# Performance work log

Measured on AMD Instinct MI355X. Metric: run time of the kernel, lower is better.

Reference implementation:

```python
import jax, jax.numpy as jnp
import numpy as np

N, E, D, R = 50000, 800000, 64, 8
NEG_SLOPE = 0.2
EPS = 1e-9


def setup_inputs() -> dict:
    key = jax.random.key(0)
    k1, k2, k3, k4, k5, k6 = jax.random.split(key, 6)
    h = jax.random.normal(k1, (N, D), dtype=jnp.float32)
    W = jax.random.normal(k2, (R, D, D), dtype=jnp.float32) / np.sqrt(D)
    a = jax.random.normal(k3, (R, 2 * D), dtype=jnp.float32) * 0.1
    dropout_mask = jnp.ones((D,), dtype=jnp.float32)
    src = jax.random.randint(k4, (E,), 0, N, dtype=jnp.int32)
    dst = jax.random.randint(k5, (E,), 0, N, dtype=jnp.int32)
    etype = jax.random.randint(k6, (E,), 0, R, dtype=jnp.int32)
    return {"h": h, "W": W, "a": a, "dropout_mask": dropout_mask,
            "src": src, "dst": dst, "etype": etype}


def reference(h, W, a, dropout_mask, src, dst, etype):
    # message_func: relation-specific transform of source node states.
    # Compute h @ W_r for all relations once ([R,N,D]), then gather per edge.
    hW = jnp.einsum('nd,rde->rne', h, W)          # [R, N, D]
    msg = hW[etype, src]                           # [E, D] gather
    # attention logits: a_r . [h_dst, msg], leaky relu
    e = (jnp.sum(h[dst] * a[etype, :D], axis=-1)
         + jnp.sum(msg * a[etype, D:], axis=-1))   # [E]
    e = jnp.where(e > 0, e, NEG_SLOPE * e)
    # reduce_func: segment softmax over incoming edges per dst node
    m = jax.ops.segment_max(e, dst, num_segments=N)          # [N]
    w = jnp.exp(e - m[dst])                                   # [E]
    denom = jax.ops.segment_sum(w, dst, num_segments=N)      # [N]
    red = jax.ops.segment_sum(w[:, None] * msg, dst, num_segments=N)  # [N, D]
    red = red / (denom[:, None] + EPS)
    # apply_node_func: residual update modulated by shared dropout_mask buffer
    return h + red * dropout_mask
```

## Files before the change

### kernel.cpp

```cpp
#include <hip/hip_runtime.h>
#include <cstdint>
#include <cstddef>

#define N_NODES 50000
#define N_EDGES 800000
#define NE4 (N_EDGES / 4)
#define DIM 64
#define NREL 8
#define NBLK 782
#define NPAD (NBLK * 64)
#define NBUCK 196
#define NCHUNK 196
#define CHUNK4 1024
#define NP (NBUCK * NCHUNK)
#define NSCAN 151

typedef unsigned short u16;
typedef unsigned int u32;
typedef float f32x4 __attribute__((ext_vector_type(4)));
typedef short bf16x8 __attribute__((ext_vector_type(8)));

__device__ __forceinline__ u16 f2b(float f) {
  union { float f; u32 u; } c; c.f = f;
  u32 u = c.u;
  return (u16)((u + 0x7fffu + ((u >> 16) & 1u)) >> 16);
}
__device__ __forceinline__ float b2f(u16 v) {
  union { u32 u; float f; } c; c.u = ((u32)v) << 16;
  return c.f;
}

__global__ __launch_bounds__(256) void k_phase1(const int* __restrict__ dst,
                                                const float* __restrict__ W,
                                                const float* __restrict__ a,
                                                int* __restrict__ pcnt,
                                                u16* __restrict__ WbT,
                                                u16* __restrict__ Tb) {
  __shared__ int cnt[256];
  const int t = threadIdx.x;
  if (blockIdx.x < NCHUNK) {
    const int c = blockIdx.x;
    cnt[t] = 0;
    __syncthreads();
    const int base4 = c * CHUNK4;
    const int end4 = (base4 + CHUNK4 < NE4) ? base4 + CHUNK4 : NE4;
    for (int i = base4 + t; i < end4; i += 256) {
      int4 d4 = ((const int4*)dst)[i];
      atomicAdd(&cnt[d4.x >> 8], 1);
      atomicAdd(&cnt[d4.y >> 8], 1);
      atomicAdd(&cnt[d4.z >> 8], 1);
      atomicAdd(&cnt[d4.w >> 8], 1);
    }
    __syncthreads();
    if (t < NBUCK) pcnt[t * NCHUNK + c] = cnt[t];
  } else {
    const int r = blockIdx.x - NCHUNK;
    for (int idx = t; idx < DIM * DIM; idx += 256) {
      int d = idx >> 6, k = idx & 63;
      WbT[((size_t)r * DIM + d) * DIM + k] = f2b(W[((size_t)r * DIM + k) * DIM + d]);
    }
    if (t < DIM) {
      int d = t;
      const float* Wr = W + (size_t)r * DIM * DIM + (size_t)d * DIM;
      const float* ar = a + (size_t)r * 2 * DIM + DIM;
      float acc = 0.f;
      #pragma unroll
      for (int e = 0; e < DIM; ++e) acc += Wr[e] * ar[e];
      Tb[(8 + r) * DIM + d] = f2b(acc);
      Tb[r * DIM + d] = f2b(a[r * 2 * DIM + d]);
    }
  }
}

__global__ __launch_bounds__(256) void k_phase2(const float* __restrict__ h,
                                                const u16* __restrict__ Tb,
                                                const int* __restrict__ pcnt,
                                                u16* __restrict__ hb,
                                                float* __restrict__ tbl,
                                                int* __restrict__ gbase,
                                                int* __restrict__ bsum) {
  __shared__ int lds[256];
  const int t = threadIdx.x;
  if (blockIdx.x < NBLK) {
    const int wv = t >> 6;
    const int lane = t & 63;
    const int l15 = lane & 15;
    const int kg = lane >> 4;
    const int n = blockIdx.x * 64 + wv * 16 + l15;
    const int nn = (n < N_NODES) ? n : N_NODES - 1;
    const float4* hr = (const float4*)(h + (size_t)nn * DIM);
    const float4 a0 = hr[kg * 2], a1 = hr[kg * 2 + 1];
    const float4 a2 = hr[8 + kg * 2], a3 = hr[8 + kg * 2 + 1];
    union { bf16x8 v; u32 w[4]; } b0, b1;
    b0.w[0] = (u32)f2b(a0.x) | ((u32)f2b(a0.y) << 16);
    b0.w[1] = (u32)f2b(a0.z) | ((u32)f2b(a0.w) << 16);
    b0.w[2] = (u32)f2b(a1.x) | ((u32)f2b(a1.y) << 16);
    b0.w[3] = (u32)f2b(a1.z) | ((u32)f2b(a1.w) << 16);
    b1.w[0] = (u32)f2b(a2.x) | ((u32)f2b(a2.y) << 16);
    b1.w[1] = (u32)f2b(a2.z) | ((u32)f2b(a2.w) << 16);
    b1.w[2] = (u32)f2b(a3.x) | ((u32)f2b(a3.y) << 16);
    b1.w[3] = (u32)f2b(a3.z) | ((u32)f2b(a3.w) << 16);
    const bool ok = (n < N_NODES);
    if (ok) {
      *(bf16x8*)(hb + (size_t)n * DIM + kg * 8) = b0.v;
      *(bf16x8*)(hb + (size_t)n * DIM + 32 + kg * 8) = b1.v;
    }
    const bf16x8* trow = (const bf16x8*)(Tb + (size_t)l15 * DIM);
    f32x4 acc = {0.f, 0.f, 0.f, 0.f};
    acc = __builtin_amdgcn_mfma_f32_16x16x32_bf16(trow[kg], b0.v, acc, 0, 0, 0);
    acc = __builtin_amdgcn_mfma_f32_16x16x32_bf16(trow[4 + kg], b1.v, acc, 0, 0, 0);
    if (ok) *(f32x4*)(tbl + (size_t)n * 16 + kg * 4) = acc;
  } else {
    const int sid = blockIdx.x - NBLK;
    const int i = sid * 256 + t;
    const int v = (i < NP) ? pcnt[i] : 0;
    lds[t] = v;
    __syncthreads();
    #pragma unroll
    for (int off = 1; off < 256; off <<= 1) {
      int tv = (t >= off) ? lds[t - off] : 0;
      __syncthreads();
      lds[t] += tv;
      __syncthreads();
    }
    if (i < NP) gbase[i] = lds[t] - v;
    if (t == 255) bsum[sid] = lds[255];
  }
}

__global__ void k_scanB(const int* __restrict__ bsum, int* __restrict__ boff,
                        int* __restrict__ rowstart) {
  __shared__ int lds[256];
  int t = threadIdx.x;
  int v = (t < NSCAN) ? bsum[t] : 0;
  lds[t] = v;
  __syncthreads();
  #pragma unroll
  for (int off = 1; off < 256; off <<= 1) {
    int tv = (t >= off) ? lds[t - off] : 0;
    __syncthreads();
    lds[t] += tv;
    __syncthreads();
  }
  if (t < NSCAN) boff[t] = lds[t] - v;
  if (t == 0) rowstart[N_NODES] = N_EDGES;
}

__global__ __launch_bounds__(256) void k_phase4(const int* __restrict__ src,
                                                const int* __restrict__ dst,
                                                const int* __restrict__ et,
                                                const int* __restrict__ gbase,
                                                const int* __restrict__ boff,
                                                u32* __restrict__ tmp,
                                                const u16* __restrict__ hb,
                                                const u16* __restrict__ WbT,
                                                u16* __restrict__ hW) {
  __shared__ int cur[256];
  const int t = threadIdx.x;
  if (blockIdx.x < NCHUNK) {
    const int c = blockIdx.x;
    if (t < NBUCK) {
      const int idx = t * NCHUNK + c;
      cur[t] = gbase[idx] + boff[idx >> 8];
    }
    __syncthreads();
    const int base4 = c * CHUNK4;
    const int end4 = (base4 + CHUNK4 < NE4) ? base4 + CHUNK4 : NE4;
    for (int i = base4 + t; i < end4; i += 256) {
      int4 s4 = ((const int4*)src)[i];
      int4 d4 = ((const int4*)dst)[i];
      int4 t4 = ((const int4*)et)[i];
      int p0 = atomicAdd(&cur[d4.x >> 8], 1);
      int p1 = atomicAdd(&cur[d4.y >> 8], 1);
      int p2 = atomicAdd(&cur[d4.z >> 8], 1);
      int p3 = atomicAdd(&cur[d4.w >> 8], 1);
      tmp[p0] = (u32)s4.x | ((u32)t4.x << 16) | ((u32)(d4.x & 255) << 24);
      tmp[p1] = (u32)s4.y | ((u32)t4.y << 16) | ((u32)(d4.y & 255) << 24);
      tmp[p2] = (u32)s4.z | ((u32)t4.z << 16) | ((u32)(d4.z & 255) << 24);
      tmp[p3] = (u32)s4.w | ((u32)t4.w << 16) | ((u32)(d4.w & 255) << 24);
    }
  } else {
    const int bid = blockIdx.x - NCHUNK;
    const int wv = t >> 6;
    const int lane = t & 63;
    const int l15 = lane & 15;
    const int kg = lane >> 4;
    const int n = bid * 64 + wv * 16 + l15;
    const bf16x8* hrow = (const bf16x8*)(hb + (size_t)n * DIM);
    const bf16x8 b0 = hrow[kg];
    const bf16x8 b1 = hrow[4 + kg];
    const bool ok = (n < N_NODES);
    #pragma unroll
    for (int r = 0; r < NREL; ++r) {
      #pragma unroll
      for (int dt = 0; dt < 4; ++dt) {
        const int d = dt * 16 + l15;
        const bf16x8* wrow = (const bf16x8*)(WbT + ((size_t)r * DIM + d) * DIM);
        f32x4 acc = {0.f, 0.f, 0.f, 0.f};
        acc = __builtin_amdgcn_mfma_f32_16x16x32_bf16(wrow[kg], b0, acc, 0, 0, 0);
        acc = __builtin_amdgcn_mfma_f32_16x16x32_bf16(wrow[4 + kg], b1, acc, 0, 0, 0);
        if (ok) {
          uint2 s;
          s.x = (u32)f2b(acc[0]) | ((u32)f2b(acc[1]) << 16);
          s.y = (u32)f2b(acc[2]) | ((u32)f2b(acc[3]) << 16);
          *(uint2*)(hW + ((size_t)r * N_NODES + n) * DIM + dt * 16 + kg * 4) = s;
        }
      }
    }
  }
}

__global__ __launch_bounds__(256) void k_local(const u32* __restrict__ tmp,
                                               const int* __restrict__ gbase,
                                               const int* __restrict__ boff,
                                               int* __restrict__ rowstart,
                                               int* __restrict__ epk) {
  __shared__ int hist[256];
  __shared__ int excl[256];
  __shared__ int cur[256];
  const int b = blockIdx.x;
  const int t = threadIdx.x;
  const int i0 = b * NCHUNK;
  const int base = gbase[i0] + boff[i0 >> 8];
  const int end = (b == NBUCK - 1)
                      ? N_EDGES
                      : (gbase[i0 + NCHUNK] + boff[(i0 + NCHUNK) >> 8]);
  hist[t] = 0;
  cur[t] = 0;
  __syncthreads();
  for (int i = base + t; i < end; i += 256) atomicAdd(&hist[tmp[i] >> 24], 1);
  __syncthreads();
  int v = hist[t];
  excl[t] = v;
  __syncthreads();
  #pragma unroll
  for (int off = 1; off < 256; off <<= 1) {
    int tv = (t >= off) ? excl[t - off] : 0;
    __syncthreads();
    excl[t] += tv;
    __syncthreads();
  }
  int myexcl = excl[t] - v;
  excl[t] = myexcl;
  int n = b * 256 + t;
  if (n < N_NODES) rowstart[n] = base + myexcl;
  __syncthreads();
  for (int i = base + t; i < end; i += 256) {
    u32 p = tmp[i];
    int lo = p >> 24;
    int o = atomicAdd(&cur[lo], 1);
    epk[base + excl[lo] + o] = (int)(p & 0x7ffffu);
  }
}

__global__ void k_fused(const float* __restrict__ h, const u16* __restrict__ hW,
                        const float* __restrict__ tbl,
                        const int* __restrict__ rowstart, const int* __restrict__ epk,
                        const float* __restrict__ dmask, float* __restrict__ out) {
  const int node = blockIdx.x * 4 + (threadIdx.x >> 6);
  const int lane = threadIdx.x & 63;
  const int g = lane >> 2;
  const int l = lane & 3;
  const int s = rowstart[node];
  const int e = rowstart[node + 1];
  float acc[16];
  #pragma unroll
  for (int i = 0; i < 16; ++i) acc[i] = 0.f;
  float den = 0.f;
  for (int j = s; j < e; j += 16) {
    const int idx = j + g;
    const bool valid = idx < e;
    const int p = valid ? epk[idx] : 0;
    const int sv = p & 0xffff;
    const int rv = (p >> 16) & 7;
    float lg = tbl[(size_t)node * 16 + rv] + tbl[(size_t)sv * 16 + 8 + rv];
    lg = lg > 0.f ? lg : 0.2f * lg;
    const float w = valid ? __expf(lg) : 0.f;
    den += w;
    uint4 q0 = {0u, 0u, 0u, 0u}, q1 = {0u, 0u, 0u, 0u};
    if (valid) {
      const u16* row = hW + ((size_t)rv * N_NODES + sv) * DIM + l * 16;
      q0 = *(const uint4*)row;
      q1 = *(const uint4*)(row + 8);
    }
    const u32 qa[8] = {q0.x, q0.y, q0.z, q0.w, q1.x, q1.y, q1.z, q1.w};
    #pragma unroll
    for (int c = 0; c < 8; ++c) {
      acc[2 * c]     += w * b2f((u16)(qa[c] & 0xffff));
      acc[2 * c + 1] += w * b2f((u16)(qa[c] >> 16));
    }
  }
  #pragma unroll
  for (int m = 4; m <= 32; m <<= 1) {
    den += __shfl_xor(den, m, 64);
    #pragma unroll
    for (int i = 0; i < 16; ++i) acc[i] += __shfl_xor(acc[i], m, 64);
  }
  if (lane < 4) {
    const float inv = 1.f / (den + 1e-9f);
    #pragma unroll
    for (int c = 0; c < 4; ++c) {
      const float4 hv = *(const float4*)(h + (size_t)node * DIM + l * 16 + c * 4);
      const float4 dm = *(const float4*)(dmask + l * 16 + c * 4);
      float4 o;
      o.x = hv.x + acc[c * 4 + 0] * inv * dm.x;
      o.y = hv.y + acc[c * 4 + 1] * inv * dm.y;
      o.z = hv.z + acc[c * 4 + 2] * inv * dm.z;
      o.w = hv.w + acc[c * 4 + 3] * inv * dm.w;
      *(float4*)(out + (size_t)node * DIM + l * 16 + c * 4) = o;
    }
  }
}

extern "C" void kernel_launch(void* const* d_in, const int* in_sizes, int n_in,
                              void* d_out, int out_size, void* d_ws, size_t ws_size,
                              hipStream_t stream) {
  const float* h = (const float*)d_in[0];
  const float* W = (const float*)d_in[1];
  const float* a = (const float*)d_in[2];
  const float* dmask = (const float*)d_in[3];
  const int* src = (const int*)d_in[4];
  const int* dst = (const int*)d_in[5];
  const int* et = (const int*)d_in[6];
  float* out = (float*)d_out;

  char* ws = (char*)d_ws;
  size_t off = 0;
  auto alloc = [&](size_t bytes) {
    void* p = ws + off;
    off += (bytes + 255) & ~(size_t)255;
    return p;
  };
  u16* hWbuf = (u16*)alloc((size_t)NREL * N_NODES * DIM * 2);
  u16* hb = (u16*)alloc((size_t)NPAD * DIM * 2);
  u16* WbT = (u16*)alloc((size_t)NREL * DIM * DIM * 2);
  u16* Tb = (u16*)alloc(16 * DIM * 2);
  float* tbl = (float*)alloc((size_t)N_NODES * 16 * 4);
  int* rowstart = (int*)alloc((N_NODES + 1) * 4);
  int* pcnt = (int*)alloc(NP * 4);
  int* gbase = (int*)alloc(NP * 4);
  int* bsum = (int*)alloc(NSCAN * 4);
  int* boff = (int*)alloc(NSCAN * 4);
  u32* tmp = (u32*)alloc((size_t)N_EDGES * 4);
  int* epk = (int*)alloc((size_t)(N_EDGES + 64) * 4);
  (void)off; (void)ws_size;

  k_phase1<<<NCHUNK + NREL, 256, 0, stream>>>(dst, W, a, pcnt, WbT, Tb);
  k_phase2<<<NBLK + NSCAN, 256, 0, stream>>>(h, Tb, pcnt, hb, tbl, gbase, bsum);
  k_scanB<<<1, 256, 0, stream>>>(bsum, boff, rowstart);
  k_phase4<<<NCHUNK + NBLK, 256, 0, stream>>>(src, dst, et, gbase, boff, tmp, hb,
                                              WbT, hWbuf);
  k_local<<<NBUCK, 256, 0, stream>>>(tmp, gbase, boff, rowstart, epk);
  k_fused<<<N_NODES / 4, 256, 0, stream>>>(h, hWbuf, tbl, rowstart, epk, dmask, out);
}
```

Measured before the change: 108.0 us.

## Fold block-offset scan into consumers, use nontemporal stores, narrow per-edge lane groups

Measured after the change: 114.4 us. +6.0%, slower.

```diff
diff --git a/kernel.cpp b/kernel.cpp
--- a/kernel.cpp
+++ b/kernel.cpp
@@ -19,6 +19,7 @@
 typedef unsigned int u32;
 typedef float f32x4 __attribute__((ext_vector_type(4)));
 typedef short bf16x8 __attribute__((ext_vector_type(8)));
+typedef unsigned int u32x2 __attribute__((ext_vector_type(2)));
 
 __device__ __forceinline__ u16 f2b(float f) {
   union { float f; u32 u; } c; c.f = f;
@@ -128,40 +129,39 @@
   }
 }
 
-__global__ void k_scanB(const int* __restrict__ bsum, int* __restrict__ boff,
-                        int* __restrict__ rowstart) {
-  __shared__ int lds[256];
-  int t = threadIdx.x;
-  int v = (t < NSCAN) ? bsum[t] : 0;
-  lds[t] = v;
-  __syncthreads();
-  #pragma unroll
-  for (int off = 1; off < 256; off <<= 1) {
-    int tv = (t >= off) ? lds[t - off] : 0;
-    __syncthreads();
-    lds[t] += tv;
-    __syncthreads();
-  }
-  if (t < NSCAN) boff[t] = lds[t] - v;
-  if (t == 0) rowstart[N_NODES] = N_EDGES;
-}
-
-__global__ __launch_bounds__(256) void k_phase4(const int* __restrict__ src,
+__global__ __launch_bounds__(256) void k_phase3(const int* __restrict__ src,
                                                 const int* __restrict__ dst,
                                                 const int* __restrict__ et,
                                                 const int* __restrict__ gbase,
-                                                const int* __restrict__ boff,
+                                                const int* __restrict__ bsum,
                                                 u32* __restrict__ tmp,
                                                 const u16* __restrict__ hb,
                                                 const u16* __restrict__ WbT,
                                                 u16* __restrict__ hW) {
+  __shared__ int boffs[256];
   __shared__ int cur[256];
   const int t = threadIdx.x;
   if (blockIdx.x < NCHUNK) {
     const int c = blockIdx.x;
+    {
+      int v = (t < NSCAN) ? bsum[t] : 0;
+      boffs[t] = v;
+      __syncthreads();
+      #pragma unroll
+      for (int off = 1; off < 256; off <<= 1) {
+        int tv = (t >= off) ? boffs[t - off] : 0;
+        __syncthreads();
+        boffs[t] += tv;
+        __syncthreads();
+      }
+      int ex = boffs[t] - v;
+      __syncthreads();
+      boffs[t] = ex;
+      __syncthreads();
+    }
     if (t < NBUCK) {
       const int idx = t * NCHUNK + c;
-      cur[t] = gbase[idx] + boff[idx >> 8];
+      cur[t] = gbase[idx] + boffs[idx >> 8];
     }
     __syncthreads();
     const int base4 = c * CHUNK4;
@@ -200,10 +200,11 @@
         acc = __builtin_amdgcn_mfma_f32_16x16x32_bf16(wrow[kg], b0, acc, 0, 0, 0);
         acc = __builtin_amdgcn_mfma_f32_16x16x32_bf16(wrow[4 + kg], b1, acc, 0, 0, 0);
         if (ok) {
-          uint2 s;
+          u32x2 s;
           s.x = (u32)f2b(acc[0]) | ((u32)f2b(acc[1]) << 16);
           s.y = (u32)f2b(acc[2]) | ((u32)f2b(acc[3]) << 16);
-          *(uint2*)(hW + ((size_t)r * N_NODES + n) * DIM + dt * 16 + kg * 4) = s;
+          __builtin_nontemporal_store(
+              s, (u32x2*)(hW + ((size_t)r * N_NODES + n) * DIM + dt * 16 + kg * 4));
         }
       }
     }
@@ -212,19 +213,36 @@
 
 __global__ __launch_bounds__(256) void k_local(const u32* __restrict__ tmp,
                                                const int* __restrict__ gbase,
-                                               const int* __restrict__ boff,
+                                               const int* __restrict__ bsum,
                                                int* __restrict__ rowstart,
                                                int* __restrict__ epk) {
+  __shared__ int boffs[256];
   __shared__ int hist[256];
   __shared__ int excl[256];
   __shared__ int cur[256];
   const int b = blockIdx.x;
   const int t = threadIdx.x;
+  {
+    int v = (t < NSCAN) ? bsum[t] : 0;
+    boffs[t] = v;
+    __syncthreads();
+    #pragma unroll
+    for (int off = 1; off < 256; off <<= 1) {
+      int tv = (t >= off) ? boffs[t - off] : 0;
+      __syncthreads();
+      boffs[t] += tv;
+      __syncthreads();
+    }
+    int ex = boffs[t] - v;
+    __syncthreads();
+    boffs[t] = ex;
+    __syncthreads();
+  }
   const int i0 = b * NCHUNK;
-  const int base = gbase[i0] + boff[i0 >> 8];
+  const int base = gbase[i0] + boffs[i0 >> 8];
   const int end = (b == NBUCK - 1)
                       ? N_EDGES
-                      : (gbase[i0 + NCHUNK] + boff[(i0 + NCHUNK) >> 8]);
+                      : (gbase[i0 + NCHUNK] + boffs[(i0 + NCHUNK) >> 8]);
   hist[t] = 0;
   cur[t] = 0;
   __syncthreads();
@@ -244,6 +262,7 @@
   excl[t] = myexcl;
   int n = b * 256 + t;
   if (n < N_NODES) rowstart[n] = base + myexcl;
+  if (b == NBUCK - 1 && t == 0) rowstart[N_NODES] = N_EDGES;
   __syncthreads();
   for (int i = base + t; i < end; i += 256) {
     u32 p = tmp[i];
@@ -259,15 +278,15 @@
                         const float* __restrict__ dmask, float* __restrict__ out) {
   const int node = blockIdx.x * 4 + (threadIdx.x >> 6);
   const int lane = threadIdx.x & 63;
-  const int g = lane >> 2;
-  const int l = lane & 3;
+  const int g = lane >> 3;
+  const int l = lane & 7;
   const int s = rowstart[node];
   const int e = rowstart[node + 1];
-  float acc[16];
+  float acc[8];
   #pragma unroll
-  for (int i = 0; i < 16; ++i) acc[i] = 0.f;
+  for (int i = 0; i < 8; ++i) acc[i] = 0.f;
   float den = 0.f;
-  for (int j = s; j < e; j += 16) {
+  for (int j = s; j < e; j += 8) {
     const int idx = j + g;
     const bool valid = idx < e;
     const int p = valid ? epk[idx] : 0;
@@ -277,38 +296,42 @@
     lg = lg > 0.f ? lg : 0.2f * lg;
     const float w = valid ? __expf(lg) : 0.f;
     den += w;
-    uint4 q0 = {0u, 0u, 0u, 0u}, q1 = {0u, 0u, 0u, 0u};
-    if (valid) {
-      const u16* row = hW + ((size_t)rv * N_NODES + sv) * DIM + l * 16;
-      q0 = *(const uint4*)row;
-      q1 = *(const uint4*)(row + 8);
-    }
-    const u32 qa[8] = {q0.x, q0.y, q0.z, q0.w, q1.x, q1.y, q1.z, q1.w};
-    #pragma unroll
-    for (int c = 0; c < 8; ++c) {
-      acc[2 * c]     += w * b2f((u16)(qa[c] & 0xffff));
-      acc[2 * c + 1] += w * b2f((u16)(qa[c] >> 16));
-    }
+    uint4 q = {0u, 0u, 0u, 0u};
+    if (valid) q = *(const uint4*)(hW + ((size_t)rv * N_NODES + sv) * DIM + l * 8);
+    acc[0] += w * b2f((u16)(q.x & 0xffff));
+    acc[1] += w * b2f((u16)(q.x >> 16));
+    acc[2] += w * b2f((u16)(q.y & 0xffff));
+    acc[3] += w * b2f((u16)(q.y >> 16));
+    acc[4] += w * b2f((u16)(q.z & 0xffff));
+    acc[5] += w * b2f((u16)(q.z >> 16));
+    acc[6] += w * b2f((u16)(q.w & 0xffff));
+    acc[7] += w * b2f((u16)(q.w >> 16));
   }
   #pragma unroll
-  for (int m = 4; m <= 32; m <<= 1) {
+  for (int m = 8; m <= 32; m <<= 1) {
     den += __shfl_xor(den, m, 64);
     #pragma unroll
-    for (int i = 0; i < 16; ++i) acc[i] += __shfl_xor(acc[i], m, 64);
-  }
-  if (lane < 4) {
+    for (int i = 0; i < 8; ++i) acc[i] += __shfl_xor(acc[i], m, 64);
+  }
+  if (lane < 8) {
     const float inv = 1.f / (den + 1e-9f);
-    #pragma unroll
-    for (int c = 0; c < 4; ++c) {
-      const float4 hv = *(const float4*)(h + (size_t)node * DIM + l * 16 + c * 4);
-      const float4 dm = *(const float4*)(dmask + l * 16 + c * 4);
-      float4 o;
-      o.x = hv.x + acc[c * 4 + 0] * inv * dm.x;
-      o.y = hv.y + acc[c * 4 + 1] * inv * dm.y;
-      o.z = hv.z + acc[c * 4 + 2] * inv * dm.z;
-      o.w = hv.w + acc[c * 4 + 3] * inv * dm.w;
-      *(float4*)(out + (size_t)node * DIM + l * 16 + c * 4) = o;
-    }
+    const f32x4 hv0 = __builtin_nontemporal_load(
+        (const f32x4*)(h + (size_t)node * DIM + l * 8));
+    const f32x4 hv1 = __builtin_nontemporal_load(
+        (const f32x4*)(h + (size_t)node * DIM + l * 8 + 4));
+    const float4 dm0 = *(const float4*)(dmask + l * 8);
+    const float4 dm1 = *(const float4*)(dmask + l * 8 + 4);
+    f32x4 o0, o1;
+    o0[0] = hv0[0] + acc[0] * inv * dm0.x;
+    o0[1] = hv0[1] + acc[1] * inv * dm0.y;
+    o0[2] = hv0[2] + acc[2] * inv * dm0.z;
+    o0[3] = hv0[3] + acc[3] * inv * dm0.w;
+    o1[0] = hv1[0] + acc[4] * inv * dm1.x;
+    o1[1] = hv1[1] + acc[5] * inv * dm1.y;
+    o1[2] = hv1[2] + acc[6] * inv * dm1.z;
+    o1[3] = hv1[3] + acc[7] * inv * dm1.w;
+    __builtin_nontemporal_store(o0, (f32x4*)(out + (size_t)node * DIM + l * 8));
+    __builtin_nontemporal_store(o1, (f32x4*)(out + (size_t)node * DIM + l * 8 + 4));
   }
 }
 
@@ -340,16 +363,14 @@
   int* pcnt = (int*)alloc(NP * 4);
   int* gbase = (int*)alloc(NP * 4);
   int* bsum = (int*)alloc(NSCAN * 4);
-  int* boff = (int*)alloc(NSCAN * 4);
   u32* tmp = (u32*)alloc((size_t)N_EDGES * 4);
   int* epk = (int*)alloc((size_t)(N_EDGES + 64) * 4);
   (void)off; (void)ws_size;
 
   k_phase1<<<NCHUNK + NREL, 256, 0, stream>>>(dst, W, a, pcnt, WbT, Tb);
   k_phase2<<<NBLK + NSCAN, 256, 0, stream>>>(h, Tb, pcnt, hb, tbl, gbase, bsum);
-  k_scanB<<<1, 256, 0, stream>>>(bsum, boff, rowstart);
-  k_phase4<<<NCHUNK + NBLK, 256, 0, stream>>>(src, dst, et, gbase, boff, tmp, hb,
+  k_phase3<<<NCHUNK + NBLK, 256, 0, stream>>>(src, dst, et, gbase, bsum, tmp, hb,
                                               WbT, hWbuf);
-  k_local<<<NBUCK, 256, 0, stream>>>(tmp, gbase, boff, rowstart, epk);
+  k_local<<<NBUCK, 256, 0, stream>>>(tmp, gbase, bsum, rowstart, epk);
   k_fused<<<N_NODES / 4, 256, 0, stream>>>(h, hWbuf, tbl, rowstart, epk, dmask, out);
 }
```
